# Optimization experiments

Hardware: AMD Instinct MI355X
Metric: run time of the kernel (lower is better)

## Reference

```python
import jax, jax.numpy as jnp
import numpy as np
from functools import partial

TAU = 2.0          # leak
VTH = 1.0          # threshold_value
DECAY = 1.0 - 1.0 / TAU  # decay_input=False, v_reset=0: v = v*(1-1/tau) + x
PAD = 3
STRIDE = 1


def heaviside(x):
    # forward of spikingjelly surrogate.ATan (surrogate only changes backward)
    return (x >= 0).astype(x.dtype)


def lif(v, inp):
    """One LIF step: charge, fire, hard reset (v_reset=0)."""
    v = v * DECAY + inp
    s = heaviside(v - VTH)
    v = v * (1.0 - s)
    return v, s


def setup_inputs() -> dict:
    key = jax.random.key(0)
    k1, k2, k3, k4 = jax.random.split(key, 4)
    B, L = 64, 2048
    C, H, NC, K = 128, 256, 10, 7
    x = jax.random.normal(k1, (B, L), dtype=jnp.float32)
    conv_w = jax.random.normal(k2, (C, 1, K), dtype=jnp.float32) * (1.0 / np.sqrt(K))
    W1 = jax.random.normal(k3, (H, C), dtype=jnp.float32) * (1.0 / np.sqrt(C))
    W2 = jax.random.normal(k4, (NC, H), dtype=jnp.float32) * (1.0 / np.sqrt(H))
    return {"x": x, "conv_w": conv_w, "W1": W1, "W2": W2}


def _forward(x, conv_w, W1, W2):
    B = x.shape[0]
    C, H, NC = conv_w.shape[0], W1.shape[0], W2.shape[0]
    # Conv1d(1 -> C): [B, 1, L] -> [B, C, T]
    xc = jax.lax.conv_general_dilated(
        x[:, None, :], conv_w, window_strides=(STRIDE,),
        padding=[(PAD, PAD)], dimension_numbers=("NCH", "OIH", "NCH"))
    T = xc.shape[2]
    xt = jnp.transpose(xc, (2, 0, 1))  # [T, B, C]

    def step(carry, x_t):
        v1, v2, v3, acc = carry
        v1, s1 = lif(v1, x_t)                       # conv LIF  [B, C]
        v2, s2 = lif(v2, s1 @ W1.T)                 # hidden LIF [B, H]
        v3, s3 = lif(v3, s2 @ W2.T)                 # output LIF [B, NC]
        return (v1, v2, v3, acc + s3), None

    zeros = lambda d: jnp.zeros((B, d), dtype=x.dtype)
    init = (zeros(C), zeros(H), zeros(NC), zeros(NC))
    (_, _, _, acc), _ = jax.lax.scan(step, init, xt)
    return acc / T


def reference(x, conv_w, W1, W2):
    return _forward(x, conv_w, W1, W2)
```

## Files before the change

### kernel.cpp

```cpp
#include <hip/hip_runtime.h>
#include <stdint.h>

#define T_STEPS 2048
#define BB 64
#define CC 128
#define HH 256
#define NCLS 10

#define S1_OFF  0
#define DP_OFF  16777216
#define DP2_OFF 16908288
#define S2W_OFF 16924672

typedef int v4i __attribute__((ext_vector_type(4)));

__global__ __launch_bounds__(128) void k01_prep(
    const float* __restrict__ x, const float* __restrict__ cw,
    const float* __restrict__ W1, const float* __restrict__ W2,
    unsigned char* __restrict__ s1, signed char* __restrict__ dp,
    signed char* __restrict__ dp2, float* __restrict__ out) {
  const int bx = blockIdx.x;
  const int tidx = threadIdx.x;

  __shared__ float xs[200];

  if (bx < 1024) {
    const int c = tidx;
    const int b = bx & 63;
    const int t0 = (bx >> 6) * 128;
    const int ts = t0 - 64;

    const float* xb = x + b * 2048;
    for (int i = tidx; i < 200; i += 128) {
      int l = t0 - 67 + i;
      xs[i] = (l >= 0 && l < 2048) ? xb[l] : 0.0f;
    }
    __syncthreads();

    float w[7];
#pragma unroll
    for (int k = 0; k < 7; ++k) w[k] = cw[c * 7 + k];

    float xw[7];
#pragma unroll
    for (int k = 0; k < 7; ++k) xw[k] = xs[k];

    float v = 0.0f;
#pragma unroll 7
    for (int i = 0; i < 192; ++i) {
      float u = fmaf(w[0], xw[0],
                fmaf(w[1], xw[1],
                fmaf(w[2], xw[2],
                fmaf(w[3], xw[3],
                fmaf(w[4], xw[4],
                fmaf(w[5], xw[5], w[6] * xw[6]))))));
      v = fmaf(v, 0.5f, u);
      bool sp = (v >= 1.0f);
      if (i >= 64) {
        int t = ts + i;
        s1[((size_t)t * BB + b) * CC + c] = (unsigned char)(sp ? 1 : 0);
      }
      if (sp) v = 0.0f;
#pragma unroll
      for (int k = 0; k < 6; ++k) xw[k] = xw[k + 1];
      xw[6] = xs[i + 7];
    }
  } else if (bx < 1280) {
    const int h = bx - 1024;
    const int c = tidx;
    float w = W1[h * CC + c];
    int q = __float2int_rn(w * 2147483648.0f);
#pragma unroll
    for (int d = 0; d < 3; ++d) {
      int dig = (int)(signed char)(q & 0xff);
      dp[d * (HH * CC) + h * CC + c] = (signed char)dig;
      q = (q - dig) >> 8;
    }
    dp[3 * (HH * CC) + h * CC + c] = (signed char)q;
  } else if (bx < 1296) {
    const int nc = bx - 1280;
#pragma unroll
    for (int half = 0; half < 2; ++half) {
      int cc = half * 128 + tidx;
      float w = (nc < NCLS) ? W2[nc * HH + cc] : 0.0f;
      int q = __float2int_rn(w * 2147483648.0f);
#pragma unroll
      for (int d = 0; d < 3; ++d) {
        int dig = (int)(signed char)(q & 0xff);
        dp2[d * (16 * HH) + nc * HH + cc] = (signed char)dig;
        q = (q - dig) >> 8;
      }
      dp2[3 * (16 * HH) + nc * HH + cc] = (signed char)q;
    }
  } else {
#pragma unroll
    for (int i = 0; i < 5; ++i) out[tidx + 128 * i] = 0.0f;
  }
}

__global__ __launch_bounds__(256) void k2_mfma_lif2(
    const unsigned char* __restrict__ s1, const signed char* __restrict__ dp,
    unsigned int* __restrict__ s2w) {
  const int tid  = threadIdx.x;
  const int lane = tid & 63;
  const int wv   = tid >> 6;
  const int hg   = blockIdx.x;
  const int b    = blockIdx.y;
  const int chunk= blockIdx.z;
  const int t0   = chunk * 128;
  const int nwarm= (chunk == 0) ? 0 : 4;
  const int ts   = t0 - nwarm * 16;
  const int l15  = lane & 15;
  const int lg   = lane >> 4;
  const int nn   = lg >> 1;
  const int hb   = hg * 128 + wv * 32;

  v4i Bf[2][4][2];
#pragma unroll
  for (int n = 0; n < 2; ++n)
#pragma unroll
    for (int d = 0; d < 4; ++d)
#pragma unroll
      for (int kc = 0; kc < 2; ++kc)
        Bf[n][d][kc] = *(const v4i*)(dp + d * (HH * CC) +
                                     (hb + n * 16 + l15) * CC + kc * 64 + lg * 16);

  const unsigned char* ap =
      s1 + ((size_t)(ts + l15) * BB + b) * CC + lg * 16;
  v4i Af0 = *(const v4i*)(ap);
  v4i Af1 = *(const v4i*)(ap + 64);
  ap += 16 * BB * CC;

  const int a4 = l15 * 4;
  float v = 0.0f;

  const int nsub = nwarm + 8;
  for (int s = 0; s < nsub; ++s) {
    const int tb = ts + s * 16;

    v4i Pf0 = *(const v4i*)(ap);
    v4i Pf1 = *(const v4i*)(ap + 64);
    ap += 16 * BB * CC;

    float u0[4], u1[4];
#pragma unroll
    for (int n = 0; n < 2; ++n) {
      v4i a0 = {0, 0, 0, 0}, a1 = {0, 0, 0, 0}, a2 = {0, 0, 0, 0}, a3 = {0, 0, 0, 0};
      a0 = __builtin_amdgcn_mfma_i32_16x16x64_i8(Af0, Bf[n][0][0], a0, 0, 0, 0);
      a1 = __builtin_amdgcn_mfma_i32_16x16x64_i8(Af0, Bf[n][1][0], a1, 0, 0, 0);
      a2 = __builtin_amdgcn_mfma_i32_16x16x64_i8(Af0, Bf[n][2][0], a2, 0, 0, 0);
      a3 = __builtin_amdgcn_mfma_i32_16x16x64_i8(Af0, Bf[n][3][0], a3, 0, 0, 0);
      a0 = __builtin_amdgcn_mfma_i32_16x16x64_i8(Af1, Bf[n][0][1], a0, 0, 0, 0);
      a1 = __builtin_amdgcn_mfma_i32_16x16x64_i8(Af1, Bf[n][1][1], a1, 0, 0, 0);
      a2 = __builtin_amdgcn_mfma_i32_16x16x64_i8(Af1, Bf[n][2][1], a2, 0, 0, 0);
      a3 = __builtin_amdgcn_mfma_i32_16x16x64_i8(Af1, Bf[n][3][1], a3, 0, 0, 0);
#pragma unroll
      for (int r = 0; r < 4; ++r) {
        int hi = a3[r] * 256 + a2[r];
        int lo = a1[r] * 256 + a0[r];
        float u = fmaf((float)hi, 0x1p-15f, (float)lo * 0x1p-31f);
        if (n == 0) u0[r] = u; else u1[r] = u;
      }
    }

    float ua[16];
#pragma unroll
    for (int q = 0; q < 4; ++q) {
      const int addr = a4 + q * 64;
#pragma unroll
      for (int r = 0; r < 4; ++r) {
        int g0 = __builtin_amdgcn_ds_bpermute(addr, __float_as_int(u0[r]));
        int g1 = __builtin_amdgcn_ds_bpermute(addr, __float_as_int(u1[r]));
        ua[q * 4 + r] = __int_as_float(nn ? g1 : g0);
      }
    }

    unsigned sel = 0;
#pragma unroll
    for (int j = 0; j < 16; ++j) {
      v = fmaf(v, 0.5f, ua[j]);
      bool sp = (v >= 1.0f);
      if (sp) v = 0.0f;
      unsigned long long Bm = __ballot(sp);
      if (l15 == j)
        sel = (unsigned)(Bm & 0xFFFFull) |
              ((unsigned)((Bm >> 32) & 0xFFFFull) << 16);
    }

    if (s >= nwarm && lg == 0)
      s2w[((size_t)(tb + l15) * BB + b) * 8 + hg * 4 + wv] = sel;

    Af0 = Pf0; Af1 = Pf1;
  }
}

__global__ __launch_bounds__(64) void k34_gemm3_lif3(
    const unsigned int* __restrict__ s2w, const signed char* __restrict__ dp2,
    float* __restrict__ out) {
  const int lane = threadIdx.x;
  const int l15  = lane & 15;
  const int lg   = lane >> 4;
  const int b    = blockIdx.x;
  const int chunk= blockIdx.y;
  const int t0   = chunk * 32;
  const int nwarm= (chunk == 0) ? 0 : 4;
  const int ts   = t0 - nwarm * 16;

  v4i Bf[4][4];
#pragma unroll
  for (int d = 0; d < 4; ++d)
#pragma unroll
    for (int kc = 0; kc < 4; ++kc)
      Bf[d][kc] = *(const v4i*)(dp2 + d * (16 * HH) + l15 * HH + kc * 64 + lg * 16);

  const uint4* rp = (const uint4*)s2w + ((size_t)(ts + l15) * BB + b) * 2;
  uint4 r0 = rp[0], r1 = rp[1];
  rp += 16 * BB * 2;

  const int a4 = l15 * 4;
  const int hw = (lg & 1) * 16;
  float v = 0.0f, cnt = 0.0f;

  const int nsub = nwarm + 2;
  for (int s = 0; s < nsub; ++s) {
    uint4 p0 = rp[0], p1 = rp[1];
    rp += 16 * BB * 2;

    unsigned rowd[8] = {r0.x, r0.y, r0.z, r0.w, r1.x, r1.y, r1.z, r1.w};

    v4i a0 = {0, 0, 0, 0}, a1 = {0, 0, 0, 0}, a2 = {0, 0, 0, 0}, a3 = {0, 0, 0, 0};
#pragma unroll
    for (int kc = 0; kc < 4; ++kc) {
      unsigned h16 = (rowd[kc * 2 + (lg >> 1)] >> hw) & 0xFFFFu;
      v4i Af;
      Af[0] = (int)(((h16 & 0xFu) * 0x00204081u) & 0x01010101u);
      Af[1] = (int)((((h16 >> 4) & 0xFu) * 0x00204081u) & 0x01010101u);
      Af[2] = (int)((((h16 >> 8) & 0xFu) * 0x00204081u) & 0x01010101u);
      Af[3] = (int)((((h16 >> 12) & 0xFu) * 0x00204081u) & 0x01010101u);
      a0 = __builtin_amdgcn_mfma_i32_16x16x64_i8(Af, Bf[0][kc], a0, 0, 0, 0);
      a1 = __builtin_amdgcn_mfma_i32_16x16x64_i8(Af, Bf[1][kc], a1, 0, 0, 0);
      a2 = __builtin_amdgcn_mfma_i32_16x16x64_i8(Af, Bf[2][kc], a2, 0, 0, 0);
      a3 = __builtin_amdgcn_mfma_i32_16x16x64_i8(Af, Bf[3][kc], a3, 0, 0, 0);
    }

    float u[4];
#pragma unroll
    for (int r = 0; r < 4; ++r) {
      int hi = a3[r] * 256 + a2[r];
      int lo = a1[r] * 256 + a0[r];
      u[r] = fmaf((float)hi, 0x1p-15f, (float)lo * 0x1p-31f);
    }

    float ua[16];
#pragma unroll
    for (int q = 0; q < 4; ++q) {
      const int addr = a4 + q * 64;
#pragma unroll
      for (int r = 0; r < 4; ++r)
        ua[q * 4 + r] = __int_as_float(
            __builtin_amdgcn_ds_bpermute(addr, __float_as_int(u[r])));
    }

    float inc = (s >= nwarm) ? 1.0f : 0.0f;
#pragma unroll
    for (int j = 0; j < 16; ++j) {
      v = fmaf(v, 0.5f, ua[j]);
      bool sp = (v >= 1.0f);
      if (sp) { v = 0.0f; cnt += inc; }
    }

    r0 = p0; r1 = p1;
  }

  if (lane < NCLS)
    atomicAdd(&out[b * NCLS + lane], cnt * (1.0f / 2048.0f));
}

extern "C" void kernel_launch(void* const* d_in, const int* in_sizes, int n_in,
                              void* d_out, int out_size, void* d_ws, size_t ws_size,
                              hipStream_t stream) {
  const float* x  = (const float*)d_in[0];
  const float* cw = (const float*)d_in[1];
  const float* W1 = (const float*)d_in[2];
  const float* W2 = (const float*)d_in[3];
  float* out = (float*)d_out;

  char* ws = (char*)d_ws;
  unsigned char* s1  = (unsigned char*)(ws + S1_OFF);
  signed char*   dp  = (signed char*)(ws + DP_OFF);
  signed char*   dp2 = (signed char*)(ws + DP2_OFF);
  unsigned int*  s2w = (unsigned int*)(ws + S2W_OFF);

  k01_prep<<<dim3(1297), 128, 0, stream>>>(x, cw, W1, W2, s1, dp, dp2, out);
  k2_mfma_lif2<<<dim3(2, 64, 16), 256, 0, stream>>>(s1, dp, s2w);
  k34_gemm3_lif3<<<dim3(64, 64), 64, 0, stream>>>(s2w, dp2, out);
  (void)in_sizes; (void)n_in; (void)out_size; (void)ws_size;
}
```

Before: 155.7 us.

## Fuse three kernels into one persistent kernel with software grid barriers

Merges the prep/conv-LIF, hidden GEMM+LIF and output GEMM+LIF kernels into a single 1024-block launch separated by atomic-counter grid barriers, plus a memset to clear the counters. The stage-2 time chunking doubles (256 steps per block, fewer warm-up recomputations) to fit the fixed grid. This aims to remove launch gaps and tail effects between kernels, but relies on all 1024 blocks being co-resident and adds spin-wait barrier cost. Weight quantization now runs on the idle upper half of the conv blocks.

```diff
diff --git a/kernel.cpp b/kernel.cpp
--- a/kernel.cpp
+++ b/kernel.cpp
@@ -11,269 +11,287 @@
 #define DP_OFF  16777216
 #define DP2_OFF 16908288
 #define S2W_OFF 16924672
+#define BAR_OFF 21118976
 
 typedef int v4i __attribute__((ext_vector_type(4)));
 
-__global__ __launch_bounds__(128) void k01_prep(
+#define NBLK 1024u
+
+__device__ __forceinline__ void grid_barrier(unsigned* cnt) {
+  __syncthreads();
+  if (threadIdx.x == 0) {
+    __threadfence();
+    __hip_atomic_fetch_add(cnt, 1u, __ATOMIC_RELEASE, __HIP_MEMORY_SCOPE_AGENT);
+    while (__hip_atomic_load(cnt, __ATOMIC_ACQUIRE, __HIP_MEMORY_SCOPE_AGENT) <
+           NBLK) {
+      __builtin_amdgcn_s_sleep(2);
+    }
+    __threadfence();
+  }
+  __syncthreads();
+}
+
+__global__ __launch_bounds__(256, 4) void snn_fused(
     const float* __restrict__ x, const float* __restrict__ cw,
     const float* __restrict__ W1, const float* __restrict__ W2,
     unsigned char* __restrict__ s1, signed char* __restrict__ dp,
-    signed char* __restrict__ dp2, float* __restrict__ out) {
-  const int bx = blockIdx.x;
-  const int tidx = threadIdx.x;
-
-  __shared__ float xs[200];
-
-  if (bx < 1024) {
-    const int c = tidx;
-    const int b = bx & 63;
+    signed char* __restrict__ dp2, unsigned int* __restrict__ s2w,
+    unsigned* __restrict__ bar, float* __restrict__ out) {
+  const int bx  = blockIdx.x;
+  const int tid = threadIdx.x;
+
+  {
+    __shared__ float xs[200];
+    const int b  = bx & 63;
     const int t0 = (bx >> 6) * 128;
-    const int ts = t0 - 64;
-
     const float* xb = x + b * 2048;
-    for (int i = tidx; i < 200; i += 128) {
-      int l = t0 - 67 + i;
-      xs[i] = (l >= 0 && l < 2048) ? xb[l] : 0.0f;
+    if (tid < 128) {
+      for (int i = tid; i < 200; i += 128) {
+        int l = t0 - 67 + i;
+        xs[i] = (l >= 0 && l < 2048) ? xb[l] : 0.0f;
+      }
     }
     __syncthreads();
 
-    float w[7];
-#pragma unroll
-    for (int k = 0; k < 7; ++k) w[k] = cw[c * 7 + k];
-
-    float xw[7];
-#pragma unroll
-    for (int k = 0; k < 7; ++k) xw[k] = xs[k];
-
-    float v = 0.0f;
+    if (tid < 128) {
+      const int c  = tid;
+      const int ts = t0 - 64;
+      float w[7];
+#pragma unroll
+      for (int k = 0; k < 7; ++k) w[k] = cw[c * 7 + k];
+      float xw[7];
+#pragma unroll
+      for (int k = 0; k < 7; ++k) xw[k] = xs[k];
+      float v = 0.0f;
 #pragma unroll 7
-    for (int i = 0; i < 192; ++i) {
-      float u = fmaf(w[0], xw[0],
-                fmaf(w[1], xw[1],
-                fmaf(w[2], xw[2],
-                fmaf(w[3], xw[3],
-                fmaf(w[4], xw[4],
-                fmaf(w[5], xw[5], w[6] * xw[6]))))));
-      v = fmaf(v, 0.5f, u);
-      bool sp = (v >= 1.0f);
-      if (i >= 64) {
-        int t = ts + i;
-        s1[((size_t)t * BB + b) * CC + c] = (unsigned char)(sp ? 1 : 0);
-      }
-      if (sp) v = 0.0f;
-#pragma unroll
-      for (int k = 0; k < 6; ++k) xw[k] = xw[k + 1];
-      xw[6] = xs[i + 7];
-    }
-  } else if (bx < 1280) {
-    const int h = bx - 1024;
-    const int c = tidx;
-    float w = W1[h * CC + c];
-    int q = __float2int_rn(w * 2147483648.0f);
-#pragma unroll
-    for (int d = 0; d < 3; ++d) {
-      int dig = (int)(signed char)(q & 0xff);
-      dp[d * (HH * CC) + h * CC + c] = (signed char)dig;
-      q = (q - dig) >> 8;
-    }
-    dp[3 * (HH * CC) + h * CC + c] = (signed char)q;
-  } else if (bx < 1296) {
-    const int nc = bx - 1280;
-#pragma unroll
-    for (int half = 0; half < 2; ++half) {
-      int cc = half * 128 + tidx;
-      float w = (nc < NCLS) ? W2[nc * HH + cc] : 0.0f;
+      for (int i = 0; i < 192; ++i) {
+        float u = fmaf(w[0], xw[0],
+                  fmaf(w[1], xw[1],
+                  fmaf(w[2], xw[2],
+                  fmaf(w[3], xw[3],
+                  fmaf(w[4], xw[4],
+                  fmaf(w[5], xw[5], w[6] * xw[6]))))));
+        v = fmaf(v, 0.5f, u);
+        bool sp = (v >= 1.0f);
+        if (i >= 64) {
+          int t = ts + i;
+          s1[((size_t)t * BB + b) * CC + c] = (unsigned char)(sp ? 1 : 0);
+        }
+        if (sp) v = 0.0f;
+#pragma unroll
+        for (int k = 0; k < 6; ++k) xw[k] = xw[k + 1];
+        xw[6] = xs[i + 7];
+      }
+    } else if (bx < 256) {
+      const int h = bx, c = tid - 128;
+      float w = W1[h * CC + c];
       int q = __float2int_rn(w * 2147483648.0f);
 #pragma unroll
       for (int d = 0; d < 3; ++d) {
         int dig = (int)(signed char)(q & 0xff);
-        dp2[d * (16 * HH) + nc * HH + cc] = (signed char)dig;
+        dp[d * (HH * CC) + h * CC + c] = (signed char)dig;
         q = (q - dig) >> 8;
       }
-      dp2[3 * (16 * HH) + nc * HH + cc] = (signed char)q;
-    }
-  } else {
-#pragma unroll
-    for (int i = 0; i < 5; ++i) out[tidx + 128 * i] = 0.0f;
+      dp[3 * (HH * CC) + h * CC + c] = (signed char)q;
+    } else if (bx < 272) {
+      const int nc = bx - 256;
+#pragma unroll
+      for (int half = 0; half < 2; ++half) {
+        int cc = half * 128 + (tid - 128);
+        float w = (nc < NCLS) ? W2[nc * HH + cc] : 0.0f;
+        int q = __float2int_rn(w * 2147483648.0f);
+#pragma unroll
+        for (int d = 0; d < 3; ++d) {
+          int dig = (int)(signed char)(q & 0xff);
+          dp2[d * (16 * HH) + nc * HH + cc] = (signed char)dig;
+          q = (q - dig) >> 8;
+        }
+        dp2[3 * (16 * HH) + nc * HH + cc] = (signed char)q;
+      }
+    } else if (bx == 272) {
+      const int i = tid - 128;
+#pragma unroll
+      for (int k = 0; k < 5; ++k) out[i + 128 * k] = 0.0f;
+    }
   }
-}
-
-__global__ __launch_bounds__(256) void k2_mfma_lif2(
-    const unsigned char* __restrict__ s1, const signed char* __restrict__ dp,
-    unsigned int* __restrict__ s2w) {
-  const int tid  = threadIdx.x;
-  const int lane = tid & 63;
-  const int wv   = tid >> 6;
-  const int hg   = blockIdx.x;
-  const int b    = blockIdx.y;
-  const int chunk= blockIdx.z;
-  const int t0   = chunk * 128;
-  const int nwarm= (chunk == 0) ? 0 : 4;
-  const int ts   = t0 - nwarm * 16;
-  const int l15  = lane & 15;
-  const int lg   = lane >> 4;
-  const int nn   = lg >> 1;
-  const int hb   = hg * 128 + wv * 32;
-
-  v4i Bf[2][4][2];
-#pragma unroll
-  for (int n = 0; n < 2; ++n)
+
+  grid_barrier(bar);
+
+  {
+    const int lane = tid & 63;
+    const int wv   = tid >> 6;
+    const int hg   = bx >> 9;
+    const int b    = (bx >> 3) & 63;
+    const int chunk= bx & 7;
+    const int t0   = chunk * 256;
+    const int nwarm= (chunk == 0) ? 0 : 4;
+    const int ts   = t0 - nwarm * 16;
+    const int l15  = lane & 15;
+    const int lg   = lane >> 4;
+    const int nn   = lg >> 1;
+    const int hb   = hg * 128 + wv * 32;
+
+    v4i Bf[2][4][2];
+#pragma unroll
+    for (int n = 0; n < 2; ++n)
+#pragma unroll
+      for (int d = 0; d < 4; ++d)
+#pragma unroll
+        for (int kc = 0; kc < 2; ++kc)
+          Bf[n][d][kc] = *(const v4i*)(dp + d * (HH * CC) +
+                                       (hb + n * 16 + l15) * CC + kc * 64 + lg * 16);
+
+    const unsigned char* ap =
+        s1 + ((size_t)(ts + l15) * BB + b) * CC + lg * 16;
+    v4i Af0 = *(const v4i*)(ap);
+    v4i Af1 = *(const v4i*)(ap + 64);
+    ap += 16 * BB * CC;
+
+    const int a4 = l15 * 4;
+    float v = 0.0f;
+
+    const int nsub = nwarm + 16;
+    for (int s = 0; s < nsub; ++s) {
+      const int tb = ts + s * 16;
+
+      v4i Pf0 = *(const v4i*)(ap);
+      v4i Pf1 = *(const v4i*)(ap + 64);
+      ap += 16 * BB * CC;
+
+      float u0[4], u1[4];
+#pragma unroll
+      for (int n = 0; n < 2; ++n) {
+        v4i a0 = {0, 0, 0, 0}, a1 = {0, 0, 0, 0}, a2 = {0, 0, 0, 0}, a3 = {0, 0, 0, 0};
+        a0 = __builtin_amdgcn_mfma_i32_16x16x64_i8(Af0, Bf[n][0][0], a0, 0, 0, 0);
+        a1 = __builtin_amdgcn_mfma_i32_16x16x64_i8(Af0, Bf[n][1][0], a1, 0, 0, 0);
+        a2 = __builtin_amdgcn_mfma_i32_16x16x64_i8(Af0, Bf[n][2][0], a2, 0, 0, 0);
+        a3 = __builtin_amdgcn_mfma_i32_16x16x64_i8(Af0, Bf[n][3][0], a3, 0, 0, 0);
+        a0 = __builtin_amdgcn_mfma_i32_16x16x64_i8(Af1, Bf[n][0][1], a0, 0, 0, 0);
+        a1 = __builtin_amdgcn_mfma_i32_16x16x64_i8(Af1, Bf[n][1][1], a1, 0, 0, 0);
+        a2 = __builtin_amdgcn_mfma_i32_16x16x64_i8(Af1, Bf[n][2][1], a2, 0, 0, 0);
+        a3 = __builtin_amdgcn_mfma_i32_16x16x64_i8(Af1, Bf[n][3][1], a3, 0, 0, 0);
+#pragma unroll
+        for (int r = 0; r < 4; ++r) {
+          int hi = a3[r] * 256 + a2[r];
+          int lo = a1[r] * 256 + a0[r];
+          float u = fmaf((float)hi, 0x1p-15f, (float)lo * 0x1p-31f);
+          if (n == 0) u0[r] = u; else u1[r] = u;
+        }
+      }
+
+      float ua[16];
+#pragma unroll
+      for (int q = 0; q < 4; ++q) {
+        const int addr = a4 + q * 64;
+#pragma unroll
+        for (int r = 0; r < 4; ++r) {
+          int g0 = __builtin_amdgcn_ds_bpermute(addr, __float_as_int(u0[r]));
+          int g1 = __builtin_amdgcn_ds_bpermute(addr, __float_as_int(u1[r]));
+          ua[q * 4 + r] = __int_as_float(nn ? g1 : g0);
+        }
+      }
+
+      unsigned sel = 0;
+#pragma unroll
+      for (int j = 0; j < 16; ++j) {
+        v = fmaf(v, 0.5f, ua[j]);
+        bool sp = (v >= 1.0f);
+        if (sp) v = 0.0f;
+        unsigned long long Bm = __ballot(sp);
+        if (l15 == j)
+          sel = (unsigned)(Bm & 0xFFFFull) |
+                ((unsigned)((Bm >> 32) & 0xFFFFull) << 16);
+      }
+
+      if (s >= nwarm && lg == 0)
+        s2w[((size_t)(tb + l15) * BB + b) * 8 + hg * 4 + wv] = sel;
+
+      Af0 = Pf0; Af1 = Pf1;
+    }
+  }
+
+  grid_barrier(bar + 16);
+
+  {
+    const int lane = tid & 63;
+    const int wv   = tid >> 6;
+    const int l15  = lane & 15;
+    const int lg   = lane >> 4;
+    const int b    = bx & 63;
+    const int cg   = ((bx >> 6) << 2) | wv;
+    const int t0   = cg * 32;
+    const int nwarm= (cg == 0) ? 0 : 4;
+    const int ts   = t0 - nwarm * 16;
+
+    v4i Bf[4][4];
 #pragma unroll
     for (int d = 0; d < 4; ++d)
 #pragma unroll
-      for (int kc = 0; kc < 2; ++kc)
-        Bf[n][d][kc] = *(const v4i*)(dp + d * (HH * CC) +
-                                     (hb + n * 16 + l15) * CC + kc * 64 + lg * 16);
-
-  const unsigned char* ap =
-      s1 + ((size_t)(ts + l15) * BB + b) * CC + lg * 16;
-  v4i Af0 = *(const v4i*)(ap);
-  v4i Af1 = *(const v4i*)(ap + 64);
-  ap += 16 * BB * CC;
-
-  const int a4 = l15 * 4;
-  float v = 0.0f;
-
-  const int nsub = nwarm + 8;
-  for (int s = 0; s < nsub; ++s) {
-    const int tb = ts + s * 16;
-
-    v4i Pf0 = *(const v4i*)(ap);
-    v4i Pf1 = *(const v4i*)(ap + 64);
-    ap += 16 * BB * CC;
-
-    float u0[4], u1[4];
-#pragma unroll
-    for (int n = 0; n < 2; ++n) {
+      for (int kc = 0; kc < 4; ++kc)
+        Bf[d][kc] = *(const v4i*)(dp2 + d * (16 * HH) + l15 * HH + kc * 64 + lg * 16);
+
+    const uint4* rp = (const uint4*)s2w + ((size_t)(ts + l15) * BB + b) * 2;
+    uint4 r0 = rp[0], r1 = rp[1];
+    rp += 16 * BB * 2;
+
+    const int a4 = l15 * 4;
+    const int hw = (lg & 1) * 16;
+    float v = 0.0f, cnt = 0.0f;
+
+    const int nsub = nwarm + 2;
+    for (int s = 0; s < nsub; ++s) {
+      uint4 p0 = rp[0], p1 = rp[1];
+      rp += 16 * BB * 2;
+
+      unsigned rowd[8] = {r0.x, r0.y, r0.z, r0.w, r1.x, r1.y, r1.z, r1.w};
+
       v4i a0 = {0, 0, 0, 0}, a1 = {0, 0, 0, 0}, a2 = {0, 0, 0, 0}, a3 = {0, 0, 0, 0};
-      a0 = __builtin_amdgcn_mfma_i32_16x16x64_i8(Af0, Bf[n][0][0], a0, 0, 0, 0);
-      a1 = __builtin_amdgcn_mfma_i32_16x16x64_i8(Af0, Bf[n][1][0], a1, 0, 0, 0);
-      a2 = __builtin_amdgcn_mfma_i32_16x16x64_i8(Af0, Bf[n][2][0], a2, 0, 0, 0);
-      a3 = __builtin_amdgcn_mfma_i32_16x16x64_i8(Af0, Bf[n][3][0], a3, 0, 0, 0);
-      a0 = __builtin_amdgcn_mfma_i32_16x16x64_i8(Af1, Bf[n][0][1], a0, 0, 0, 0);
-      a1 = __builtin_amdgcn_mfma_i32_16x16x64_i8(Af1, Bf[n][1][1], a1, 0, 0, 0);
-      a2 = __builtin_amdgcn_mfma_i32_16x16x64_i8(Af1, Bf[n][2][1], a2, 0, 0, 0);
-      a3 = __builtin_amdgcn_mfma_i32_16x16x64_i8(Af1, Bf[n][3][1], a3, 0, 0, 0);
+#pragma unroll
+      for (int kc = 0; kc < 4; ++kc) {
+        unsigned h16 = (rowd[kc * 2 + (lg >> 1)] >> hw) & 0xFFFFu;
+        v4i Af;
+        Af[0] = (int)(((h16 & 0xFu) * 0x00204081u) & 0x01010101u);
+        Af[1] = (int)((((h16 >> 4) & 0xFu) * 0x00204081u) & 0x01010101u);
+        Af[2] = (int)((((h16 >> 8) & 0xFu) * 0x00204081u) & 0x01010101u);
+        Af[3] = (int)((((h16 >> 12) & 0xFu) * 0x00204081u) & 0x01010101u);
+        a0 = __builtin_amdgcn_mfma_i32_16x16x64_i8(Af, Bf[0][kc], a0, 0, 0, 0);
+        a1 = __builtin_amdgcn_mfma_i32_16x16x64_i8(Af, Bf[1][kc], a1, 0, 0, 0);
+        a2 = __builtin_amdgcn_mfma_i32_16x16x64_i8(Af, Bf[2][kc], a2, 0, 0, 0);
+        a3 = __builtin_amdgcn_mfma_i32_16x16x64_i8(Af, Bf[3][kc], a3, 0, 0, 0);
+      }
+
+      float u[4];
 #pragma unroll
       for (int r = 0; r < 4; ++r) {
         int hi = a3[r] * 256 + a2[r];
         int lo = a1[r] * 256 + a0[r];
-        float u = fmaf((float)hi, 0x1p-15f, (float)lo * 0x1p-31f);
-        if (n == 0) u0[r] = u; else u1[r] = u;
-      }
-    }
-
-    float ua[16];
-#pragma unroll
-    for (int q = 0; q < 4; ++q) {
-      const int addr = a4 + q * 64;
-#pragma unroll
-      for (int r = 0; r < 4; ++r) {
-        int g0 = __builtin_amdgcn_ds_bpermute(addr, __float_as_int(u0[r]));
-        int g1 = __builtin_amdgcn_ds_bpermute(addr, __float_as_int(u1[r]));
-        ua[q * 4 + r] = __int_as_float(nn ? g1 : g0);
-      }
-    }
-
-    unsigned sel = 0;
-#pragma unroll
-    for (int j = 0; j < 16; ++j) {
-      v = fmaf(v, 0.5f, ua[j]);
-      bool sp = (v >= 1.0f);
-      if (sp) v = 0.0f;
-      unsigned long long Bm = __ballot(sp);
-      if (l15 == j)
-        sel = (unsigned)(Bm & 0xFFFFull) |
-              ((unsigned)((Bm >> 32) & 0xFFFFull) << 16);
-    }
-
-    if (s >= nwarm && lg == 0)
-      s2w[((size_t)(tb + l15) * BB + b) * 8 + hg * 4 + wv] = sel;
-
-    Af0 = Pf0; Af1 = Pf1;
+        u[r] = fmaf((float)hi, 0x1p-15f, (float)lo * 0x1p-31f);
+      }
+
+      float ua[16];
+#pragma unroll
+      for (int q = 0; q < 4; ++q) {
+        const int addr = a4 + q * 64;
+#pragma unroll
+        for (int r = 0; r < 4; ++r)
+          ua[q * 4 + r] = __int_as_float(
+              __builtin_amdgcn_ds_bpermute(addr, __float_as_int(u[r])));
+      }
+
+      float inc = (s >= nwarm) ? 1.0f : 0.0f;
+#pragma unroll
+      for (int j = 0; j < 16; ++j) {
+        v = fmaf(v, 0.5f, ua[j]);
+        bool sp = (v >= 1.0f);
+        if (sp) { v = 0.0f; cnt += inc; }
+      }
+
+      r0 = p0; r1 = p1;
+    }
+
+    if (lane < NCLS)
+      atomicAdd(&out[b * NCLS + lane], cnt * (1.0f / 2048.0f));
   }
-}
-
-__global__ __launch_bounds__(64) void k34_gemm3_lif3(
-    const unsigned int* __restrict__ s2w, const signed char* __restrict__ dp2,
-    float* __restrict__ out) {
-  const int lane = threadIdx.x;
-  const int l15  = lane & 15;
-  const int lg   = lane >> 4;
-  const int b    = blockIdx.x;
-  const int chunk= blockIdx.y;
-  const int t0   = chunk * 32;
-  const int nwarm= (chunk == 0) ? 0 : 4;
-  const int ts   = t0 - nwarm * 16;
-
-  v4i Bf[4][4];
-#pragma unroll
-  for (int d = 0; d < 4; ++d)
-#pragma unroll
-    for (int kc = 0; kc < 4; ++kc)
-      Bf[d][kc] = *(const v4i*)(dp2 + d * (16 * HH) + l15 * HH + kc * 64 + lg * 16);
-
-  const uint4* rp = (const uint4*)s2w + ((size_t)(ts + l15) * BB + b) * 2;
-  uint4 r0 = rp[0], r1 = rp[1];
-  rp += 16 * BB * 2;
-
-  const int a4 = l15 * 4;
-  const int hw = (lg & 1) * 16;
-  float v = 0.0f, cnt = 0.0f;
-
-  const int nsub = nwarm + 2;
-  for (int s = 0; s < nsub; ++s) {
-    uint4 p0 = rp[0], p1 = rp[1];
-    rp += 16 * BB * 2;
-
-    unsigned rowd[8] = {r0.x, r0.y, r0.z, r0.w, r1.x, r1.y, r1.z, r1.w};
-
-    v4i a0 = {0, 0, 0, 0}, a1 = {0, 0, 0, 0}, a2 = {0, 0, 0, 0}, a3 = {0, 0, 0, 0};
-#pragma unroll
-    for (int kc = 0; kc < 4; ++kc) {
-      unsigned h16 = (rowd[kc * 2 + (lg >> 1)] >> hw) & 0xFFFFu;
-      v4i Af;
-      Af[0] = (int)(((h16 & 0xFu) * 0x00204081u) & 0x01010101u);
-      Af[1] = (int)((((h16 >> 4) & 0xFu) * 0x00204081u) & 0x01010101u);
-      Af[2] = (int)((((h16 >> 8) & 0xFu) * 0x00204081u) & 0x01010101u);
-      Af[3] = (int)((((h16 >> 12) & 0xFu) * 0x00204081u) & 0x01010101u);
-      a0 = __builtin_amdgcn_mfma_i32_16x16x64_i8(Af, Bf[0][kc], a0, 0, 0, 0);
-      a1 = __builtin_amdgcn_mfma_i32_16x16x64_i8(Af, Bf[1][kc], a1, 0, 0, 0);
-      a2 = __builtin_amdgcn_mfma_i32_16x16x64_i8(Af, Bf[2][kc], a2, 0, 0, 0);
-      a3 = __builtin_amdgcn_mfma_i32_16x16x64_i8(Af, Bf[3][kc], a3, 0, 0, 0);
-    }
-
-    float u[4];
-#pragma unroll
-    for (int r = 0; r < 4; ++r) {
-      int hi = a3[r] * 256 + a2[r];
-      int lo = a1[r] * 256 + a0[r];
-      u[r] = fmaf((float)hi, 0x1p-15f, (float)lo * 0x1p-31f);
-    }
-
-    float ua[16];
-#pragma unroll
-    for (int q = 0; q < 4; ++q) {
-      const int addr = a4 + q * 64;
-#pragma unroll
-      for (int r = 0; r < 4; ++r)
-        ua[q * 4 + r] = __int_as_float(
-            __builtin_amdgcn_ds_bpermute(addr, __float_as_int(u[r])));
-    }
-
-    float inc = (s >= nwarm) ? 1.0f : 0.0f;
-#pragma unroll
-    for (int j = 0; j < 16; ++j) {
-      v = fmaf(v, 0.5f, ua[j]);
-      bool sp = (v >= 1.0f);
-      if (sp) { v = 0.0f; cnt += inc; }
-    }
-
-    r0 = p0; r1 = p1;
-  }
-
-  if (lane < NCLS)
-    atomicAdd(&out[b * NCLS + lane], cnt * (1.0f / 2048.0f));
 }
 
 extern "C" void kernel_launch(void* const* d_in, const int* in_sizes, int n_in,
@@ -290,9 +308,10 @@
   signed char*   dp  = (signed char*)(ws + DP_OFF);
   signed char*   dp2 = (signed char*)(ws + DP2_OFF);
   unsigned int*  s2w = (unsigned int*)(ws + S2W_OFF);
-
-  k01_prep<<<dim3(1297), 128, 0, stream>>>(x, cw, W1, W2, s1, dp, dp2, out);
-  k2_mfma_lif2<<<dim3(2, 64, 16), 256, 0, stream>>>(s1, dp, s2w);
-  k34_gemm3_lif3<<<dim3(64, 64), 64, 0, stream>>>(s2w, dp2, out);
+  unsigned*      bar = (unsigned*)(ws + BAR_OFF);
+
+  hipMemsetAsync(bar, 0, 256, stream);
+  snn_fused<<<dim3(NBLK), 256, 0, stream>>>(x, cw, W1, W2, s1, dp, dp2, s2w,
+                                            bar, out);
   (void)in_sizes; (void)n_in; (void)out_size; (void)ws_size;
 }
```

Result: slower. 461.4 us (+196.3%).
